# Performance work log

Measured on AMD Instinct MI355X. Metric: run time of the kernel, lower is better.

Reference implementation:

```python
import jax, jax.numpy as jnp
import numpy as np

LAMBDA_FGW = 0.5
TAU_KL = 0.1
N_OUTER = 5
N_SINKHORN = 10
DIM = 512


def _pdist(a, b):
    # sqrt(clamp(||a-b||^2, 1e-6)) computed via expansion (avoids BxKxMxD temp)
    n2 = ((a * a).sum(-1)[:, :, None] + (b * b).sum(-1)[:, None, :]
          - 2.0 * jnp.einsum('bkd,bmd->bkm', a, b))
    return jnp.sqrt(jnp.clip(n2, 1e-6, None))


def setup_inputs() -> dict:
    key = jax.random.key(0)
    ks = jax.random.split(key, 10)
    B, K, M, D = 256, 128, 128, DIM
    inp = {
        'sq': jax.random.normal(ks[0], (B, K, D), jnp.float32),
        'sr': jax.random.normal(ks[1], (B, M, D), jnp.float32),
        'mask_q': jax.random.uniform(ks[2], (B, K), jnp.float32),
        'mask_r': jax.random.uniform(ks[3], (B, M), jnp.float32),
        'centroids_q': jax.random.normal(ks[4], (B, K, D), jnp.float32),
        'centroids_r': jax.random.normal(ks[5], (B, M, D), jnp.float32),
        'W1': jax.random.normal(ks[6], (D, D), jnp.float32) * 0.02,
        'b1': jnp.zeros((D,), jnp.float32),
        'W2': jax.random.normal(ks[7], (D, D), jnp.float32) * 0.02,
        'b2': jnp.zeros((D,), jnp.float32),
        'log_eps': jnp.asarray(np.log(0.05), jnp.float32),
    }
    return inp


def reference(sq, sr, mask_q, mask_r, centroids_q, centroids_r, W1, b1, W2, b2, log_eps):
    proj = lambda x: jax.nn.relu(x @ W1 + b1) @ W2 + b2
    pq, pr = proj(sq), proj(sr)
    C = _pdist(pq, pr)                      # [B,K,M]
    Sq = _pdist(centroids_q, centroids_q)   # [B,K,K]
    Sr = _pdist(centroids_r, centroids_r)   # [B,M,M]

    mu = mask_q / (mask_q.sum(-1, keepdims=True) + 1e-8)  # [B,K]
    nu = mask_r / (mask_r.sum(-1, keepdims=True) + 1e-8)  # [B,M]
    T = mu[:, :, None] * nu[:, None, :]

    eps = jnp.clip(jnp.exp(log_eps), 0.01, 0.5)
    rho = TAU_KL / (TAU_KL + eps)
    log_mu = jnp.log(jnp.clip(mu, 1e-8, None))
    log_nu = jnp.log(jnp.clip(nu, 1e-8, None))
    Sq2, Sr2 = Sq * Sq, Sr * Sr

    C_fgw = C
    for _ in range(N_OUTER):
        t1 = jnp.einsum('bkl,bl->bk', Sq2, T.sum(2))[:, :, None]
        t2 = jnp.einsum('bm,bmn->bn', T.sum(1), Sr2)[:, None, :]
        L_gw = t1 + t2 - 2.0 * jnp.einsum('bkl,blm->bkm', Sq, jnp.einsum('blm,bmn->bln', T, Sr))
        C_fgw = (1.0 - LAMBDA_FGW) * C + LAMBDA_FGW * L_gw
        log_K = -C_fgw / eps
        log_u = jnp.zeros_like(mu)
        log_v = jnp.zeros_like(nu)
        for _ in range(N_SINKHORN):
            log_u = rho * (log_mu - jax.nn.logsumexp(log_K + log_v[:, None, :], axis=2))
            log_v = rho * (log_nu - jax.nn.logsumexp(log_K + log_u[:, :, None], axis=1))
        T = jnp.exp(log_u[:, :, None] + log_K + log_v[:, None, :])

    cost = (T * C_fgw).sum((-1, -2))
    similarity = jax.nn.sigmoid(-cost)
    return similarity, T, C, cost
```

## Files before the change

kernel.cpp:

```cpp
#include <hip/hip_runtime.h>
#include <math.h>

typedef unsigned short u16;
typedef __attribute__((ext_vector_type(4))) float f32x4;
typedef __attribute__((ext_vector_type(8))) short bf16x8;
typedef __attribute__((ext_vector_type(4))) unsigned short u16x4;
typedef __attribute__((ext_vector_type(8))) unsigned short u16x8;

#define DEVI static __device__ __forceinline__

DEVI float b2f(u16 u){ union{float f; unsigned i;} v; v.i = ((unsigned)u)<<16; return v.f; }
DEVI u16 f2b(float f){ union{float f; unsigned i;} v; v.f=f;
  unsigned r = v.i + 0x7fffu + ((v.i>>16)&1u); return (u16)(r>>16); }

DEVI void gload_lds16(const void* g, void* l){
  __builtin_amdgcn_global_load_lds((const __attribute__((address_space(1))) void*)g,
                                   (__attribute__((address_space(3))) void*)l, 16, 0, 0);
}

DEVI f32x4 vmax4(f32x4 a, f32x4 b){
  f32x4 r; r[0]=fmaxf(a[0],b[0]); r[1]=fmaxf(a[1],b[1]);
  r[2]=fmaxf(a[2],b[2]); r[3]=fmaxf(a[3],b[3]); return r;
}

__global__ void prepw_k(const float* __restrict__ W, u16* __restrict__ Wt){
  int id = blockIdx.x*256 + threadIdx.x;
  int k = id>>9, c = id&511;
  Wt[c*512 + k] = f2b(W[id]);
}

template<int ACT, int NORM, int AF32>
__global__ __launch_bounds__(256) void gemm_k(const u16* __restrict__ X,
    const float* __restrict__ Xf1, const float* __restrict__ Xf2,
    const u16* __restrict__ Wt, const float* __restrict__ bias, u16* __restrict__ OUT,
    float* __restrict__ NP){
  __shared__ __align__(16) u16 sA[128*64];
  __shared__ __align__(16) u16 sB[128*64];
  const int tid = threadIdx.x, wave = tid>>6, lane = tid&63;
  const int bid = (blockIdx.x&7)*256 + (blockIdx.x>>3);
  const int rblk = bid>>2, cb = (bid&3)<<7;
  const u16* Xb = AF32 ? nullptr : (X + (size_t)rblk*(128*512));
  const float* Xbf = AF32 ? (rblk<256 ? Xf1 + (size_t)rblk*65536
                                      : Xf2 + (size_t)(rblk-256)*65536) : nullptr;
  const u16* Wb = Wt + (size_t)cb*512;
  const int lrow = lane&15, lg = lane>>4, wr = wave>>1, wc = wave&1;
  f32x4 acc[4][4] = {};
  for (int s=0;s<8;s++){
    const int k0 = s<<6;
    #pragma unroll
    for (int q=0;q<4;q++){
      const int i = (wave<<2)+q;
      const int row = (i<<3) + (lane>>3);
      const int cd = (lane&7) ^ (row&7);
      if (AF32){
        const float* src = Xbf + row*512 + k0 + (cd<<3);
        const f32x4 va = *(const f32x4*)src;
        const f32x4 vb = *(const f32x4*)(src+4);
        u16x8 t;
        #pragma unroll
        for (int e=0;e<4;e++){ t[e]=f2b(va[e]); t[4+e]=f2b(vb[e]); }
        *(u16x8*)((char*)sA + i*1024 + lane*16) = t;
      } else {
        gload_lds16(Xb + row*512 + k0 + (cd<<3), sA + i*512);
      }
      gload_lds16(Wb + row*512 + k0 + (cd<<3), sB + i*512);
    }
    __syncthreads();
    #pragma unroll
    for (int kh=0;kh<2;kh++){
      bf16x8 a_[4], b_[4];
      #pragma unroll
      for (int i=0;i<4;i++){
        const int ra = (wr<<6)+(i<<4)+lrow;
        a_[i] = *(const bf16x8*)(sA + ra*64 + ((((kh<<2)+lg)^(ra&7))<<3));
        const int rb = (wc<<6)+(i<<4)+lrow;
        b_[i] = *(const bf16x8*)(sB + rb*64 + ((((kh<<2)+lg)^(rb&7))<<3));
      }
      #pragma unroll
      for (int i=0;i<4;i++)
        #pragma unroll
        for (int j=0;j<4;j++)
          acc[i][j] = __builtin_amdgcn_mfma_f32_16x16x32_bf16(a_[i], b_[j], acc[i][j], 0,0,0);
    }
    __syncthreads();
  }
  float nacc[4][4];
  if (NORM){
    #pragma unroll
    for (int i=0;i<4;i++)
      #pragma unroll
      for (int r=0;r<4;r++) nacc[i][r]=0.f;
  }
  #pragma unroll
  for (int j=0;j<4;j++){
    const int col = cb + (wc<<6) + (j<<4) + lrow;
    const float bv = bias[col];
    #pragma unroll
    for (int i=0;i<4;i++){
      const int row0 = (rblk<<7) + (wr<<6) + (i<<4) + (lg<<2);
      #pragma unroll
      for (int r=0;r<4;r++){
        float v = acc[i][j][r] + bv;
        if (ACT) v = fmaxf(v, 0.f);
        u16 pb = f2b(v);
        OUT[(size_t)(row0+r)*512 + col] = pb;
        if (NORM){ float fv = b2f(pb); nacc[i][r] += fv*fv; }
      }
    }
  }
  if (NORM){
    #pragma unroll
    for (int i=0;i<4;i++)
      #pragma unroll
      for (int r=0;r<4;r++){
        float v = nacc[i][r];
        v += __shfl_xor(v,1); v += __shfl_xor(v,2);
        v += __shfl_xor(v,4); v += __shfl_xor(v,8);
        if (lrow==0)
          atomicAdd(NP + (rblk<<7) + (wr<<6) + (i<<4) + (lg<<2) + r, v);
      }
  }
}

__global__ __launch_bounds__(256) void pdist0_k(const u16* __restrict__ Xa,
    const u16* __restrict__ Xb2, const float* __restrict__ na, const float* __restrict__ nb,
    float* __restrict__ OUT){
  __shared__ __align__(16) u16 sA[128*64];
  __shared__ __align__(16) u16 sB[128*64];
  const int tid = threadIdx.x, wave = tid>>6, lane = tid&63;
  const int b = blockIdx.x;
  const u16* Ab = Xa + (size_t)b*(128*512);
  const u16* Bb = Xb2 + (size_t)b*(128*512);
  const int lrow = lane&15, lg = lane>>4, wr = wave>>1, wc = wave&1;
  f32x4 acc[4][4] = {};
  for (int s=0;s<8;s++){
    const int k0 = s<<6;
    #pragma unroll
    for (int q=0;q<4;q++){
      const int i = (wave<<2)+q;
      const int row = (i<<3) + (lane>>3);
      const int cd = (lane&7) ^ (row&7);
      gload_lds16(Ab + row*512 + k0 + (cd<<3), sA + i*512);
      gload_lds16(Bb + row*512 + k0 + (cd<<3), sB + i*512);
    }
    __syncthreads();
    #pragma unroll
    for (int kh=0;kh<2;kh++){
      bf16x8 a_[4], b_[4];
      #pragma unroll
      for (int i=0;i<4;i++){
        const int ra = (wr<<6)+(i<<4)+lrow;
        a_[i] = *(const bf16x8*)(sA + ra*64 + ((((kh<<2)+lg)^(ra&7))<<3));
        const int rb = (wc<<6)+(i<<4)+lrow;
        b_[i] = *(const bf16x8*)(sB + rb*64 + ((((kh<<2)+lg)^(rb&7))<<3));
      }
      #pragma unroll
      for (int i=0;i<4;i++)
        #pragma unroll
        for (int j=0;j<4;j++)
          acc[i][j] = __builtin_amdgcn_mfma_f32_16x16x32_bf16(a_[i], b_[j], acc[i][j], 0,0,0);
    }
    __syncthreads();
  }
  #pragma unroll
  for (int j=0;j<4;j++){
    const int col = (wc<<6)+(j<<4)+lrow;
    const float nbv = nb[b*128+col];
    #pragma unroll
    for (int i=0;i<4;i++){
      const int row0 = (wr<<6)+(i<<4)+(lg<<2);
      #pragma unroll
      for (int r=0;r<4;r++){
        float n2 = na[b*128+row0+r] + nbv - 2.0f*acc[i][j][r];
        OUT[(size_t)b*16384 + (size_t)(row0+r)*128 + col] = sqrtf(fmaxf(n2, 1e-6f));
      }
    }
  }
}

__global__ __launch_bounds__(256) void pdistS_k(const float* __restrict__ Sf,
    char* __restrict__ SHL){
  __shared__ __align__(16) u16 sA[128*64];
  __shared__ float nrm[128];
  const int tid = threadIdx.x, wave = tid>>6, lane = tid&63;
  const int b = blockIdx.x;
  const float* Sb = Sf + (size_t)b*65536;
  const int lrow = lane&15, lg = lane>>4, wr = wave>>1, wc = wave&1;
  f32x4 acc[4][4] = {};
  float nacc[4] = {0.f,0.f,0.f,0.f};
  for (int s=0;s<8;s++){
    const int k0 = s<<6;
    #pragma unroll
    for (int q=0;q<4;q++){
      const int i = (wave<<2)+q;
      const int row = (i<<3) + (lane>>3);
      const int cd = (lane&7) ^ (row&7);
      const float* src = Sb + row*512 + k0 + (cd<<3);
      const f32x4 va = *(const f32x4*)src;
      const f32x4 vb = *(const f32x4*)(src+4);
      u16x8 t;
      #pragma unroll
      for (int e=0;e<4;e++){ t[e]=f2b(va[e]); t[4+e]=f2b(vb[e]); }
      #pragma unroll
      for (int e=0;e<8;e++){ float fv=b2f(t[e]); nacc[q]=fmaf(fv,fv,nacc[q]); }
      *(u16x8*)((char*)sA + i*1024 + lane*16) = t;
    }
    __syncthreads();
    #pragma unroll
    for (int kh=0;kh<2;kh++){
      bf16x8 a_[4], b_[4];
      #pragma unroll
      for (int i=0;i<4;i++){
        const int ra = (wr<<6)+(i<<4)+lrow;
        a_[i] = *(const bf16x8*)(sA + ra*64 + ((((kh<<2)+lg)^(ra&7))<<3));
        const int rb = (wc<<6)+(i<<4)+lrow;
        b_[i] = *(const bf16x8*)(sA + rb*64 + ((((kh<<2)+lg)^(rb&7))<<3));
      }
      #pragma unroll
      for (int i=0;i<4;i++)
        #pragma unroll
        for (int j=0;j<4;j++)
          acc[i][j] = __builtin_amdgcn_mfma_f32_16x16x32_bf16(a_[i], b_[j], acc[i][j], 0,0,0);
    }
    __syncthreads();
  }
  #pragma unroll
  for (int q=0;q<4;q++){
    float v = nacc[q];
    v += __shfl_xor(v,1); v += __shfl_xor(v,2); v += __shfl_xor(v,4);
    if ((lane&7)==0) nrm[((wave<<2)+q)*8 + (lane>>3)] = v;
  }
  __syncthreads();
  #pragma unroll
  for (int j=0;j<4;j++){
    const int col = (wc<<6)+(j<<4)+lrow;
    const float nbv = nrm[col];
    #pragma unroll
    for (int i=0;i<4;i++){
      const int row0 = (wr<<6)+(i<<4)+(lg<<2);
      u16x4 hi4, lo4;
      #pragma unroll
      for (int r=0;r<4;r++){
        float n2 = nrm[row0+r] + nbv - 2.0f*acc[i][j][r];
        float sv = sqrtf(fmaxf(n2, 1e-6f));
        u16 h = f2b(sv); hi4[r] = h;
        lo4[r] = f2b(sv - b2f(h));
      }
      const int sa = col*256 + ((((row0>>3)^col)&15)<<4) + ((row0&7)<<1);
      char* base = SHL + (size_t)b*65536;
      *(u16x4*)(base + sa) = hi4;
      *(u16x4*)(base + 32768 + sa) = lo4;
    }
  }
}

__global__ void prep_k(const float* __restrict__ mask_q, const float* __restrict__ mask_r,
                       float* __restrict__ lmu2, float* __restrict__ lnu2,
                       float* __restrict__ mu, float* __restrict__ nu){
  int b = blockIdx.x, t = threadIdx.x;
  __shared__ float red[4];
  float mq = mask_q[b*128+t], mr = mask_r[b*128+t];
  float s1 = mq, s2 = mr;
  #pragma unroll
  for (int off=1;off<64;off<<=1){ s1 += __shfl_xor(s1,off); s2 += __shfl_xor(s2,off); }
  if ((t&63)==0){ red[t>>6] = s1; red[2+(t>>6)] = s2; }
  __syncthreads();
  float sumq = red[0]+red[1], sumr = red[2]+red[3];
  float muv = mq/(sumq+1e-8f), nuv = mr/(sumr+1e-8f);
  lmu2[b*128+t] = __log2f(fmaxf(muv,1e-8f));
  lnu2[b*128+t] = __log2f(fmaxf(nuv,1e-8f));
  mu[b*128+t] = muv;
  nu[b*128+t] = nuv;
}

__global__ __launch_bounds__(512,1) void fgw_loop_k(
    const char* __restrict__ SQHL, const char* __restrict__ SRHL,
    const float* __restrict__ C_g,
    const float* __restrict__ MU, const float* __restrict__ NU,
    const float* __restrict__ LMU2, const float* __restrict__ LNU2,
    const float* __restrict__ log_eps,
    float* __restrict__ T_out, float* __restrict__ cost_out, float* __restrict__ sim_out)
{
  __shared__ __align__(16) char bufT[65536];
  __shared__ __align__(16) char bufS[65536];
  __shared__ __align__(16) float avs[128], bvs[128], t1s[128], t2s[128];
  __shared__ __align__(16) float lus[128], lvs[128];
  __shared__ float redc[8];

  const int b = blockIdx.x, tid = threadIdx.x;
  const int w = tid>>6, lane = tid&63, l15 = lane&15, lg = lane>>4;
  const char* SqHLb = SQHL + (size_t)b*65536;
  const char* SrHLb = SRHL + (size_t)b*65536;
  const float* Cb   = C_g + (size_t)b*16384;
  const float* MUb  = MU + b*128;
  const float* NUb  = NU + b*128;

  float eps = __expf(log_eps[0]); eps = fminf(fmaxf(eps,0.01f),0.5f);
  const float rho = 0.1f/(0.1f+eps);
  const float hscale = 0.5f*1.4426950408889634f/eps;

  const int kR = 16*w + l15;
  const int n0 = 16*w + 4*lg;
  const float lmu2R = LMU2[b*128+kR];
  const float lnu2C = LNU2[b*128+kR];

  const int rowA256 = (16*w + l15)*256;
  const int glo2 = lg ^ (l15 & 3);
  const int ghi2 = l15 & 12;
  const int wtail = l15*256 + ((((2*w + (lg>>1)) ^ l15)&15)<<4) + ((lg&1)<<3);

  f32x4 Cf2[8];
  #pragma unroll
  for (int kt=0;kt<8;kt++)
    Cf2[kt] = -hscale * (*(const f32x4*)(Cb + (size_t)(16*kt+l15)*128 + n0));

  f32x4 lkR[8], lkC[8];
  float luR = 0.f, lvC = 0.f;

  for (int outer=0; outer<5; outer++){
    #pragma unroll
    for (int r2=0;r2<8;r2++)
      gload_lds16(SrHLb + r2*8192 + tid*16, bufS + r2*8192 + tid*16);
    {
      f32x4 avp = {0.f,0.f,0.f,0.f};
      float bvp = 0.f;
      #pragma unroll
      for (int q=0;q<8;q++){
        f32x4 TR, TC;
        if (outer==0){
          const f32x4 nu4 = *(const f32x4*)(NUb + 16*q + 4*lg);
          const f32x4 mu4 = *(const f32x4*)(MUb + 16*q + 4*lg);
          const float muR = MUb[kR], nuC = NUb[kR];
          TR = muR*nu4; TC = mu4*nuC;
        } else {
          const f32x4 lv4 = *(const f32x4*)&lvs[16*q + 4*lg];
          const f32x4 lu4 = *(const f32x4*)&lus[16*q + 4*lg];
          #pragma unroll
          for (int e=0;e<4;e++){
            TR[e] = exp2f(lkR[q][e] + luR + lv4[e]);
            TC[e] = exp2f(lkC[q][e] + lu4[e] + lvC);
          }
        }
        u16x4 hi4, lo4;
        #pragma unroll
        for (int e=0;e<4;e++){
          u16 h = f2b(TR[e]); hi4[e] = h;
          lo4[e] = f2b(TR[e] - b2f(h));
        }
        const int sa = kR*256 + ((((2*q+(lg>>1)) ^ l15)&15)<<4) + ((lg&1)<<3);
        *(u16x4*)(bufT + sa) = hi4;
        *(u16x4*)(bufT + 32768 + sa) = lo4;
        avp += TR;
        bvp += TC[0]+TC[1]+TC[2]+TC[3];
      }
      float av = avp[0]+avp[1]+avp[2]+avp[3];
      av += __shfl_xor(av,16); av += __shfl_xor(av,32);
      bvp += __shfl_xor(bvp,16); bvp += __shfl_xor(bvp,32);
      if (lg==0){ avs[kR] = av; bvs[kR] = bvp; }
    }
    __syncthreads();

    {
      const int p = tid>>2, sub = tid&3;
      float s2 = 0.f;
      #pragma unroll
      for (int gg=0; gg<4; gg++){
        const int g = 4*sub+gg;
        const int off = p*256 + (((g ^ (p&15))&15)<<4);
        const u16x8 h8 = *(const u16x8*)(bufS + off);
        const u16x8 l8 = *(const u16x8*)(bufS + 32768 + off);
        const f32x4 bva = *(const f32x4*)&bvs[8*g];
        const f32x4 bvb = *(const f32x4*)&bvs[8*g+4];
        #pragma unroll
        for (int e=0;e<4;e++){
          float x = b2f(h8[e]) + b2f(l8[e]);
          s2 = fmaf(bva[e], x*x, s2);
          float y2 = b2f(h8[4+e]) + b2f(l8[4+e]);
          s2 = fmaf(bvb[e], y2*y2, s2);
        }
      }
      s2 += __shfl_xor(s2,1); s2 += __shfl_xor(s2,2);
      if (sub==0) t2s[p] = s2;
    }
    f32x4 acc1[8] = {};
    #pragma unroll
    for (int qt=0;qt<4;qt++){
      const int colOff = (((4*qt) ^ ghi2) | glo2) << 4;
      const bf16x8 ahi = *(const bf16x8*)(bufT + rowA256 + colOff);
      const bf16x8 alo = *(const bf16x8*)(bufT + 32768 + rowA256 + colOff);
      const int bbase = l15*256 + colOff;
      #pragma unroll
      for (int nt=0;nt<8;nt++){
        const bf16x8 bhi = *(const bf16x8*)(bufS + nt*4096 + bbase);
        const bf16x8 blo = *(const bf16x8*)(bufS + 32768 + nt*4096 + bbase);
        acc1[nt] = __builtin_amdgcn_mfma_f32_16x16x32_bf16(ahi, bhi, acc1[nt], 0,0,0);
        acc1[nt] = __builtin_amdgcn_mfma_f32_16x16x32_bf16(ahi, blo, acc1[nt], 0,0,0);
        acc1[nt] = __builtin_amdgcn_mfma_f32_16x16x32_bf16(alo, bhi, acc1[nt], 0,0,0);
      }
    }
    __syncthreads();

    #pragma unroll
    for (int r2=0;r2<8;r2++)
      gload_lds16(SqHLb + r2*8192 + tid*16, bufS + r2*8192 + tid*16);
    #pragma unroll
    for (int nt=0;nt<8;nt++){
      u16x4 hi4, lo4;
      #pragma unroll
      for (int r=0;r<4;r++){
        u16 h = f2b(acc1[nt][r]); hi4[r] = h;
        lo4[r] = f2b(acc1[nt][r] - b2f(h));
      }
      const int sa = nt*4096 + wtail;
      *(u16x4*)(bufT + sa) = hi4;
      *(u16x4*)(bufT + 32768 + sa) = lo4;
    }
    __syncthreads();

    {
      const int p = tid>>2, sub = tid&3;
      float s1 = 0.f;
      #pragma unroll
      for (int gg=0; gg<4; gg++){
        const int g = 4*sub+gg;
        const int off = p*256 + (((g ^ (p&15))&15)<<4);
        const u16x8 h8 = *(const u16x8*)(bufS + off);
        const u16x8 l8 = *(const u16x8*)(bufS + 32768 + off);
        const f32x4 ava = *(const f32x4*)&avs[8*g];
        const f32x4 avb = *(const f32x4*)&avs[8*g+4];
        #pragma unroll
        for (int e=0;e<4;e++){
          float x = b2f(h8[e]) + b2f(l8[e]);
          s1 = fmaf(ava[e], x*x, s1);
          float y2 = b2f(h8[4+e]) + b2f(l8[4+e]);
          s1 = fmaf(avb[e], y2*y2, s1);
        }
      }
      s1 += __shfl_xor(s1,1); s1 += __shfl_xor(s1,2);
      if (sub==0) t1s[p] = s1;
    }
    f32x4 acc2[8] = {};
    #pragma unroll
    for (int qt=0;qt<4;qt++){
      const int colOff = (((4*qt) ^ ghi2) | glo2) << 4;
      const bf16x8 ahi = *(const bf16x8*)(bufT + rowA256 + colOff);
      const bf16x8 alo = *(const bf16x8*)(bufT + 32768 + rowA256 + colOff);
      const int bbase = l15*256 + colOff;
      #pragma unroll
      for (int kt=0;kt<8;kt++){
        const bf16x8 bhi = *(const bf16x8*)(bufS + kt*4096 + bbase);
        const bf16x8 blo = *(const bf16x8*)(bufS + 32768 + kt*4096 + bbase);
        acc2[kt] = __builtin_amdgcn_mfma_f32_16x16x32_bf16(ahi, bhi, acc2[kt], 0,0,0);
        acc2[kt] = __builtin_amdgcn_mfma_f32_16x16x32_bf16(ahi, blo, acc2[kt], 0,0,0);
        acc2[kt] = __builtin_amdgcn_mfma_f32_16x16x32_bf16(alo, bhi, acc2[kt], 0,0,0);
      }
    }
    __syncthreads();

    f32x4 lkf[8];
    {
      const f32x4 t24 = *(const f32x4*)&t2s[n0];
      #pragma unroll
      for (int kt=0;kt<8;kt++){
        const float t1v = t1s[16*kt+l15];
        lkf[kt] = Cf2[kt] + hscale*(2.0f*acc2[kt] - t1v - t24);
      }
    }
    #pragma unroll
    for (int kt=0;kt<8;kt++){
      const int row = 16*kt + l15;
      const int gp = ((4*w+lg) ^ (row&31)) & 31;
      *(f32x4*)(bufT + row*512 + gp*16) = lkf[kt];
      #pragma unroll
      for (int e=0;e<4;e++){
        const int n = n0 + e;
        const int gt = ((4*kt + (l15>>2)) ^ (n&31)) & 31;
        *(float*)(bufS + n*512 + gt*16 + (l15&3)*4) = lkf[kt][e];
      }
    }
    __syncthreads();
    #pragma unroll
    for (int q=0;q<8;q++){
      const int g1 = ((4*q+lg) ^ (kR&31)) & 31;
      lkR[q] = *(const f32x4*)(bufT + kR*512 + g1*16);
      lkC[q] = *(const f32x4*)(bufS + kR*512 + g1*16);
    }

    for (int it=0; it<10; it++){
      f32x4 y[8];
      #pragma unroll
      for (int q=0;q<8;q++){
        y[q] = lkR[q];
        if (it) y[q] += *(const f32x4*)&lvs[16*q+4*lg];
      }
      f32x4 m4 = vmax4(vmax4(vmax4(y[0],y[1]),vmax4(y[2],y[3])),
                       vmax4(vmax4(y[4],y[5]),vmax4(y[6],y[7])));
      float mx = fmaxf(fmaxf(m4[0],m4[1]), fmaxf(m4[2],m4[3]));
      mx = fmaxf(mx,__shfl_xor(mx,16)); mx = fmaxf(mx,__shfl_xor(mx,32));
      f32x4 s4 = {0.f,0.f,0.f,0.f};
      #pragma unroll
      for (int q=0;q<8;q++){
        #pragma unroll
        for (int e=0;e<4;e++) s4[e] += exp2f(y[q][e]-mx);
      }
      float s = s4[0]+s4[1]+s4[2]+s4[3];
      s += __shfl_xor(s,16); s += __shfl_xor(s,32);
      luR = rho*(lmu2R - (mx + __log2f(s)));
      if (lg==0) lus[kR] = luR;
      __syncthreads();
      #pragma unroll
      for (int q=0;q<8;q++)
        y[q] = lkC[q] + *(const f32x4*)&lus[16*q+4*lg];
      m4 = vmax4(vmax4(vmax4(y[0],y[1]),vmax4(y[2],y[3])),
                 vmax4(vmax4(y[4],y[5]),vmax4(y[6],y[7])));
      mx = fmaxf(fmaxf(m4[0],m4[1]), fmaxf(m4[2],m4[3]));
      mx = fmaxf(mx,__shfl_xor(mx,16)); mx = fmaxf(mx,__shfl_xor(mx,32));
      s4 = (f32x4){0.f,0.f,0.f,0.f};
      #pragma unroll
      for (int q=0;q<8;q++){
        #pragma unroll
        for (int e=0;e<4;e++) s4[e] += exp2f(y[q][e]-mx);
      }
      s = s4[0]+s4[1]+s4[2]+s4[3];
      s += __shfl_xor(s,16); s += __shfl_xor(s,32);
      lvC = rho*(lnu2C - (mx + __log2f(s)));
      if (lg==0) lvs[kR] = lvC;
      __syncthreads();
    }

    if (outer==4){
      float cp = 0.f;
      float* Tb = T_out + (size_t)b*16384;
      #pragma unroll
      for (int q=0;q<8;q++){
        const f32x4 lv4 = *(const f32x4*)&lvs[16*q+4*lg];
        f32x4 t;
        #pragma unroll
        for (int e=0;e<4;e++) t[e] = exp2f(lkR[q][e] + luR + lv4[e]);
        *(f32x4*)(Tb + kR*128 + 16*q + 4*lg) = t;
        const f32x4 pr = t*lkR[q];
        cp += pr[0]+pr[1]+pr[2]+pr[3];
      }
      cp *= -eps*0.6931471805599453f;
      #pragma unroll
      for (int off=1;off<64;off<<=1) cp += __shfl_xor(cp, off);
      if (lane==0) redc[w] = cp;
      __syncthreads();
      if (tid==0){
        float tot = 0.f;
        #pragma unroll
        for (int w2=0;w2<8;w2++) tot += redc[w2];
        cost_out[b] = tot;
        sim_out[b]  = 1.0f/(1.0f + __expf(tot));
      }
    }
  }
}

extern "C" void kernel_launch(void* const* d_in, const int* in_sizes, int n_in,
                              void* d_out, int out_size, void* d_ws, size_t ws_size,
                              hipStream_t stream){
  const float* sq      = (const float*)d_in[0];
  const float* sr      = (const float*)d_in[1];
  const float* mask_q  = (const float*)d_in[2];
  const float* mask_r  = (const float*)d_in[3];
  const float* cq      = (const float*)d_in[4];
  const float* cr      = (const float*)d_in[5];
  const float* W1      = (const float*)d_in[6];
  const float* b1      = (const float*)d_in[7];
  const float* W2      = (const float*)d_in[8];
  const float* b2      = (const float*)d_in[9];
  const float* log_eps = (const float*)d_in[10];

  float* out  = (float*)d_out;
  float* sim  = out;
  float* Tm   = out + 256;
  float* Cm   = Tm + 4194304;
  float* cost = Cm + 4194304;

  char* ws = (char*)d_ws;
  size_t off = 0;
  auto alloc = [&](size_t bytes)->void*{ void* p = ws + off; off += (bytes+255)&~(size_t)255; return p; };
  u16*   PQ  = (u16*)  alloc(67108864);
  u16*   HQ  = (u16*)  alloc(67108864);
  u16*   W1T = (u16*)  alloc(524288);
  u16*   W2T = (u16*)  alloc(524288);
  float* NP  = (float*)alloc(262144);
  float* LMU = (float*)alloc(131072);
  float* LNU = (float*)alloc(131072);
  float* MUA = (float*)alloc(131072);
  float* NUA = (float*)alloc(131072);
  (void)ws_size; (void)in_sizes; (void)n_in; (void)out_size;

  char* SQHL = (char*)PQ;
  char* SRHL = (char*)PQ + 16777216;

  prepw_k<<<1024,256,0,stream>>>(W1, W1T);
  prepw_k<<<1024,256,0,stream>>>(W2, W2T);
  gemm_k<1,0,1><<<2048,256,0,stream>>>(nullptr, sq, sr, W1T, b1, HQ, nullptr);
  hipMemsetAsync(NP, 0, 262144, stream);
  gemm_k<0,1,0><<<2048,256,0,stream>>>(HQ, nullptr, nullptr, W2T, b2, PQ, NP);
  pdist0_k<<<256,256,0,stream>>>(PQ, PQ + (size_t)32768*512, NP, NP + 32768, Cm);
  pdistS_k<<<256,256,0,stream>>>(cq, SQHL);
  pdistS_k<<<256,256,0,stream>>>(cr, SRHL);
  prep_k<<<256,128,0,stream>>>(mask_q, mask_r, LMU, LNU, MUA, NUA);
  fgw_loop_k<<<256,512,0,stream>>>(SQHL, SRHL, Cm, MUA, NUA, LMU, LNU,
                                   log_eps, Tm, cost, sim);
}
```

Measured before the change: 456.6 us.

## Merge prologue kernels, derive column marginal analytically, restructure LDS transpose and barriers

Fuses weight transposes and mask normalization into one prologue kernel and both centroid pdist launches into one grid, reducing launch count. In the FGW loop, the column sums of T are computed in closed form from lvC instead of summing exp2 over TC, which removes half the exp work. The Sr hi/lo prefetch is moved so it overlaps the tail of each outer iteration. The log-kernel transpose now goes through a single buffer with a new slot layout, and the barriers are replaced by a waitcnt-plus-s_barrier asm. The risks are that the closed-form marginal relies on the Sinkhorn fixed-point identity, and that the asm barrier only waits on LDS traffic, not on outstanding global-to-LDS loads.

```diff
diff --git a/kernel.cpp b/kernel.cpp
--- a/kernel.cpp
+++ b/kernel.cpp
@@ -18,15 +18,42 @@
                                    (__attribute__((address_space(3))) void*)l, 16, 0, 0);
 }
 
+DEVI void lds_bar(){ asm volatile("s_waitcnt lgkmcnt(0)\n\ts_barrier" ::: "memory"); }
+
 DEVI f32x4 vmax4(f32x4 a, f32x4 b){
   f32x4 r; r[0]=fmaxf(a[0],b[0]); r[1]=fmaxf(a[1],b[1]);
   r[2]=fmaxf(a[2],b[2]); r[3]=fmaxf(a[3],b[3]); return r;
 }
 
-__global__ void prepw_k(const float* __restrict__ W, u16* __restrict__ Wt){
-  int id = blockIdx.x*256 + threadIdx.x;
-  int k = id>>9, c = id&511;
-  Wt[c*512 + k] = f2b(W[id]);
+__global__ void prologue_k(const float* __restrict__ W1, const float* __restrict__ W2,
+                           u16* __restrict__ W1T, u16* __restrict__ W2T,
+                           const float* __restrict__ mask_q, const float* __restrict__ mask_r,
+                           float* __restrict__ lmu2, float* __restrict__ lnu2,
+                           float* __restrict__ mu, float* __restrict__ nu){
+  const int blk = blockIdx.x;
+  if (blk < 2048){
+    const float* W = (blk<1024)? W1 : W2;
+    u16* Wt = (blk<1024)? W1T : W2T;
+    int id = (blk&1023)*256 + threadIdx.x;
+    int k = id>>9, c = id&511;
+    Wt[c*512 + k] = f2b(W[id]);
+  } else {
+    __shared__ float red[2][4];
+    const int h = threadIdx.x>>7, t = threadIdx.x&127;
+    const int b = (blk-2048)*2 + h;
+    float mq = mask_q[b*128+t], mr = mask_r[b*128+t];
+    float s1 = mq, s2 = mr;
+    #pragma unroll
+    for (int off=1;off<64;off<<=1){ s1 += __shfl_xor(s1,off); s2 += __shfl_xor(s2,off); }
+    if ((t&63)==0){ red[h][(t>>6)&1] = s1; red[h][2+((t>>6)&1)] = s2; }
+    __syncthreads();
+    float sumq = red[h][0]+red[h][1], sumr = red[h][2]+red[h][3];
+    float muv = mq/(sumq+1e-8f), nuv = mr/(sumr+1e-8f);
+    lmu2[b*128+t] = __log2f(fmaxf(muv,1e-8f));
+    lnu2[b*128+t] = __log2f(fmaxf(nuv,1e-8f));
+    mu[b*128+t] = muv;
+    nu[b*128+t] = nuv;
+  }
 }
 
 template<int ACT, int NORM, int AF32>
@@ -178,13 +205,14 @@
   }
 }
 
-__global__ __launch_bounds__(256) void pdistS_k(const float* __restrict__ Sf,
-    char* __restrict__ SHL){
+__global__ __launch_bounds__(256) void pdistS2_k(const float* __restrict__ cq,
+    const float* __restrict__ cr, char* __restrict__ SQHL, char* __restrict__ SRHL){
   __shared__ __align__(16) u16 sA[128*64];
   __shared__ float nrm[128];
   const int tid = threadIdx.x, wave = tid>>6, lane = tid&63;
-  const int b = blockIdx.x;
-  const float* Sb = Sf + (size_t)b*65536;
+  const int b = blockIdx.x & 255;
+  const float* Sb = ((blockIdx.x<256)? cq : cr) + (size_t)b*65536;
+  char* SHL = (blockIdx.x<256)? SQHL : SRHL;
   const int lrow = lane&15, lg = lane>>4, wr = wave>>1, wc = wave&1;
   f32x4 acc[4][4] = {};
   float nacc[4] = {0.f,0.f,0.f,0.f};
@@ -252,25 +280,6 @@
       *(u16x4*)(base + 32768 + sa) = lo4;
     }
   }
-}
-
-__global__ void prep_k(const float* __restrict__ mask_q, const float* __restrict__ mask_r,
-                       float* __restrict__ lmu2, float* __restrict__ lnu2,
-                       float* __restrict__ mu, float* __restrict__ nu){
-  int b = blockIdx.x, t = threadIdx.x;
-  __shared__ float red[4];
-  float mq = mask_q[b*128+t], mr = mask_r[b*128+t];
-  float s1 = mq, s2 = mr;
-  #pragma unroll
-  for (int off=1;off<64;off<<=1){ s1 += __shfl_xor(s1,off); s2 += __shfl_xor(s2,off); }
-  if ((t&63)==0){ red[t>>6] = s1; red[2+(t>>6)] = s2; }
-  __syncthreads();
-  float sumq = red[0]+red[1], sumr = red[2]+red[3];
-  float muv = mq/(sumq+1e-8f), nuv = mr/(sumr+1e-8f);
-  lmu2[b*128+t] = __log2f(fmaxf(muv,1e-8f));
-  lnu2[b*128+t] = __log2f(fmaxf(nuv,1e-8f));
-  mu[b*128+t] = muv;
-  nu[b*128+t] = nuv;
 }
 
 __global__ __launch_bounds__(512,1) void fgw_loop_k(
@@ -308,6 +317,7 @@
   const int glo2 = lg ^ (l15 & 3);
   const int ghi2 = l15 & 12;
   const int wtail = l15*256 + ((((2*w + (lg>>1)) ^ l15)&15)<<4) + ((lg&1)<<3);
+  const int slotW = lg*16 + (l15^lg);
 
   f32x4 Cf2[8];
   #pragma unroll
@@ -317,29 +327,23 @@
   f32x4 lkR[8], lkC[8];
   float luR = 0.f, lvC = 0.f;
 
+  #pragma unroll
+  for (int r2=0;r2<8;r2++)
+    gload_lds16(SrHLb + r2*8192 + tid*16, bufS + r2*8192 + tid*16);
+
   for (int outer=0; outer<5; outer++){
-    #pragma unroll
-    for (int r2=0;r2<8;r2++)
-      gload_lds16(SrHLb + r2*8192 + tid*16, bufS + r2*8192 + tid*16);
     {
       f32x4 avp = {0.f,0.f,0.f,0.f};
-      float bvp = 0.f;
       #pragma unroll
       for (int q=0;q<8;q++){
-        f32x4 TR, TC;
+        f32x4 TR;
         if (outer==0){
           const f32x4 nu4 = *(const f32x4*)(NUb + 16*q + 4*lg);
-          const f32x4 mu4 = *(const f32x4*)(MUb + 16*q + 4*lg);
-          const float muR = MUb[kR], nuC = NUb[kR];
-          TR = muR*nu4; TC = mu4*nuC;
+          TR = MUb[kR]*nu4;
         } else {
           const f32x4 lv4 = *(const f32x4*)&lvs[16*q + 4*lg];
-          const f32x4 lu4 = *(const f32x4*)&lus[16*q + 4*lg];
           #pragma unroll
-          for (int e=0;e<4;e++){
-            TR[e] = exp2f(lkR[q][e] + luR + lv4[e]);
-            TC[e] = exp2f(lkC[q][e] + lu4[e] + lvC);
-          }
+          for (int e=0;e<4;e++) TR[e] = exp2f(lkR[q][e] + luR + lv4[e]);
         }
         u16x4 hi4, lo4;
         #pragma unroll
@@ -351,12 +355,13 @@
         *(u16x4*)(bufT + sa) = hi4;
         *(u16x4*)(bufT + 32768 + sa) = lo4;
         avp += TR;
-        bvp += TC[0]+TC[1]+TC[2]+TC[3];
       }
       float av = avp[0]+avp[1]+avp[2]+avp[3];
       av += __shfl_xor(av,16); av += __shfl_xor(av,32);
-      bvp += __shfl_xor(bvp,16); bvp += __shfl_xor(bvp,32);
-      if (lg==0){ avs[kR] = av; bvs[kR] = bvp; }
+      if (lg==0){
+        avs[kR] = av;
+        bvs[kR] = (outer==0) ? NUb[kR] : exp2f(lnu2C - 10.f*eps*lvC);
+      }
     }
     __syncthreads();
 
@@ -457,6 +462,11 @@
     }
     __syncthreads();
 
+    if (outer<4){
+      #pragma unroll
+      for (int r2=0;r2<8;r2++)
+        gload_lds16(SrHLb + r2*8192 + tid*16, bufS + r2*8192 + tid*16);
+    }
     f32x4 lkf[8];
     {
       const f32x4 t24 = *(const f32x4*)&t2s[n0];
@@ -467,23 +477,19 @@
       }
     }
     #pragma unroll
-    for (int kt=0;kt<8;kt++){
-      const int row = 16*kt + l15;
-      const int gp = ((4*w+lg) ^ (row&31)) & 31;
-      *(f32x4*)(bufT + row*512 + gp*16) = lkf[kt];
+    for (int kt=0;kt<8;kt++)
+      *(f32x4*)(bufT + (((kt*8+w)*64 + slotW)<<4)) = lkf[kt];
+    lds_bar();
+    #pragma unroll
+    for (int q=0;q<8;q++)
+      lkR[q] = *(const f32x4*)(bufT + (((w*8+q)*64 + slotW)<<4));
+    #pragma unroll
+    for (int q=0;q<8;q++){
       #pragma unroll
       for (int e=0;e<4;e++){
-        const int n = n0 + e;
-        const int gt = ((4*kt + (l15>>2)) ^ (n&31)) & 31;
-        *(float*)(bufS + n*512 + gt*16 + (l15&3)*4) = lkf[kt][e];
-      }
-    }
-    __syncthreads();
-    #pragma unroll
-    for (int q=0;q<8;q++){
-      const int g1 = ((4*q+lg) ^ (kR&31)) & 31;
-      lkR[q] = *(const f32x4*)(bufT + kR*512 + g1*16);
-      lkC[q] = *(const f32x4*)(bufS + kR*512 + g1*16);
+        const int slotC = (l15>>2)*16 + ((4*lg+e) ^ (l15>>2));
+        lkC[q][e] = *(const float*)(bufT + (((q*8+w)*64 + slotC)<<4) + ((l15&3)<<2));
+      }
     }
 
     for (int it=0; it<10; it++){
@@ -507,7 +513,7 @@
       s += __shfl_xor(s,16); s += __shfl_xor(s,32);
       luR = rho*(lmu2R - (mx + __log2f(s)));
       if (lg==0) lus[kR] = luR;
-      __syncthreads();
+      lds_bar();
       #pragma unroll
       for (int q=0;q<8;q++)
         y[q] = lkC[q] + *(const f32x4*)&lus[16*q+4*lg];
@@ -525,7 +531,7 @@
       s += __shfl_xor(s,16); s += __shfl_xor(s,32);
       lvC = rho*(lnu2C - (mx + __log2f(s)));
       if (lg==0) lvs[kR] = lvC;
-      __syncthreads();
+      lds_bar();
     }
 
     if (outer==4){
@@ -595,15 +601,14 @@
   char* SQHL = (char*)PQ;
   char* SRHL = (char*)PQ + 16777216;
 
-  prepw_k<<<1024,256,0,stream>>>(W1, W1T);
-  prepw_k<<<1024,256,0,stream>>>(W2, W2T);
+  prologue_k<<<2176,256,0,stream>>>(W1, W2, W1T, W2T, mask_q, mask_r,
+                                    LMU, LNU, MUA, NUA);
   gemm_k<1,0,1><<<2048,256,0,stream>>>(nullptr, sq, sr, W1T, b1, HQ, nullptr);
   hipMemsetAsync(NP, 0, 262144, stream);
   gemm_k<0,1,0><<<2048,256,0,stream>>>(HQ, nullptr, nullptr, W2T, b2, PQ, NP);
   pdist0_k<<<256,256,0,stream>>>(PQ, PQ + (size_t)32768*512, NP, NP + 32768, Cm);
-  pdistS_k<<<256,256,0,stream>>>(cq, SQHL);
-  pdistS_k<<<256,256,0,stream>>>(cr, SRHL);
-  prep_k<<<256,128,0,stream>>>(mask_q, mask_r, LMU, LNU, MUA, NUA);
+  pdistS2_k<<<512,256,0,stream>>>(cq, cr, SQHL, SRHL);
+  prep_dummy: ;
   fgw_loop_k<<<256,512,0,stream>>>(SQHL, SRHL, Cm, MUA, NUA, LMU, LNU,
                                    log_eps, Tm, cost, sim);
 }
```

Result: faster. 435.1 us (-4.7%).
